# Kernel tuning notes

Measured on AMD Instinct MI355X. Metric: run time of the kernel, lower is better.

Reference implementation:

```python
import jax, jax.numpy as jnp
import numpy as np

B, V, K, DIN, H, DH, OBS, HID = 2048, 3, 32, 256, 8, 64, 128, 256
REP = H * DH
EPS = 1e-6


def _ln(x, g, b):
    mu = x.mean(-1, keepdims=True)
    var = ((x - mu) ** 2).mean(-1, keepdims=True)
    return (x - mu) * jax.lax.rsqrt(var + 1e-5) * g + b


def setup_inputs() -> dict:
    key = jax.random.key(0)
    ks = iter(jax.random.split(key, 32))
    nrm = lambda shape, s=0.05: jax.random.normal(next(ks), shape, jnp.float32) * s
    return {
        'x_anchor': jax.random.normal(next(ks), (B, V, DIN), jnp.float32),
        'x_neighbors': jax.random.normal(next(ks), (B, V, K, DIN), jnp.float32),
        'edge_weights': jax.random.uniform(next(ks), (B, V, K), jnp.float32),
        'g': jax.random.normal(next(ks), (B, OBS), jnp.float32),
        'aW': nrm((V, DIN, REP)), 'ab': jnp.zeros((V, REP)), 'ag': jnp.ones((V, REP)), 'abeta': jnp.zeros((V, REP)),
        'nW': nrm((V, DIN, REP)), 'nb': jnp.zeros((V, REP)), 'ng': jnp.ones((V, REP)), 'nbeta': jnp.zeros((V, REP)),
        'Wq': nrm((V, H, DH, DH)), 'Wk': nrm((V, H, DH, DH)), 'Wv': nrm((V, H, DH, DH)), 'Wo': nrm((V, H, DH, DH)),
        'geom_log_scale': jnp.zeros((V, H)),
        'cWq': nrm((H, DH, DH)), 'cWk': nrm((H, DH, DH)), 'cWv': nrm((H, DH, DH)), 'cWo': nrm((H, DH, DH)),
        'rW1': nrm((OBS, HID)), 'rb1': jnp.zeros((HID,)),
        'rW2': nrm((HID, HID)), 'rb2': jnp.zeros((HID,)),
        'vW': nrm((HID, H * V)), 'vb': jnp.zeros((H * V,)),
        'mW': nrm((HID, H)), 'mb': jnp.zeros((H,)),
        'gW': nrm((HID, H)), 'gb': jnp.zeros((H,)),
    }


def reference(x_anchor, x_neighbors, edge_weights, g, aW, ab, ag, abeta, nW, nb, ng, nbeta,
              Wq, Wk, Wv, Wo, geom_log_scale, cWq, cWk, cWv, cWo,
              rW1, rb1, rW2, rb2, vW, vb, mW, mb, gW, gb):
    # --- per-view encoders (vectorized over V with a leading v axis) ---
    ha = _ln(jnp.einsum('bvi,vio->bvo', x_anchor, aW) + ab, ag, abeta).reshape(B, V, H, DH)
    hn = _ln(jnp.einsum('bvki,vio->bvko', x_neighbors, nW) + nb[:, None, :],
             ng[:, None, :], nbeta[:, None, :]).reshape(B, V, K, H, DH)
    q = jnp.einsum('bvhd,vhde->bvhe', ha, Wq)
    k = jnp.einsum('bvkhd,vhde->bvkhe', hn, Wk)
    vv = jnp.einsum('bvkhd,vhde->bvkhe', hn, Wv)
    sc = jnp.einsum('bvhd,bvkhd->bvhk', q, k) / np.sqrt(DH).astype(np.float32)
    geom = jax.nn.softplus(geom_log_scale)  # [V,H]
    sc = sc + geom[None, :, :, None] * jnp.log(edge_weights[:, :, None, :] + EPS)
    attn = jax.nn.softmax(sc, axis=-1)
    ho = jnp.einsum('bvhk,bvkhd->bvhd', attn, vv)
    ho = jnp.einsum('bvhd,vhde->bvhe', ho, Wo) + ha  # residual
    view_tokens = jnp.transpose(ho, (0, 2, 1, 3))  # [B,H,V,Dh]
    # --- router ---
    hid = jax.nn.gelu(jnp.dot(g, rW1) + rb1, approximate=False)
    hid = jax.nn.gelu(jnp.dot(hid, rW2) + rb2, approximate=False)
    pi = jax.nn.softmax((jnp.dot(hid, vW) + vb).reshape(B, H, V), axis=-1)
    beta = jax.nn.sigmoid((jnp.dot(hid, mW) + mb)[..., None])  # [B,H,1]
    gate = jax.nn.softmax(jnp.dot(hid, gW) + gb, axis=-1)      # [B,H]
    # --- pi-weighted mixture + cross-view interaction with log-pi prior ---
    mix = jnp.einsum('bhv,bhvd->bhd', pi, view_tokens)
    qc = jnp.einsum('bhd,hde->bhe', mix, cWq)
    kc = jnp.einsum('bhvd,hde->bhve', view_tokens, cWk)
    vc = jnp.einsum('bhvd,hde->bhve', view_tokens, cWv)
    s2 = jnp.einsum('bhd,bhvd->bhv', qc, kc) / np.sqrt(DH).astype(np.float32) + jnp.log(pi + EPS)
    a2 = jax.nn.softmax(s2, axis=-1)
    cr = jnp.einsum('bhv,bhvd->bhd', a2, vc)
    cr = jnp.einsum('bhd,hde->bhe', cr, cWo)
    # mode blend + head gating; head_repr kept unflattened [B,H,Dh]
    return gate[..., None] * (beta * cr + (1.0 - beta) * mix)
```

## Files before the change

### kernel.cpp

```cpp
#include <hip/hip_runtime.h>

#define B_   2048
#define V_   3
#define K_   32
#define DIN_ 256
#define H_   8
#define DH_  64
#define REP_ 512

typedef unsigned short u16;
typedef unsigned int   u32;
typedef __bf16 bf8 __attribute__((ext_vector_type(8)));
typedef float  f4  __attribute__((ext_vector_type(4)));

static __device__ __forceinline__ u16 f2bf(float f) {
  union { float f; u32 i; } x; x.f = f;
  u32 r = (x.i + 0x7FFFu + ((x.i >> 16) & 1u)) >> 16;
  return (u16)r;
}
static __device__ __forceinline__ float bf2f(u16 u) {
  union { u32 i; float f; } x; x.i = ((u32)u) << 16;
  return x.f;
}

__global__ __launch_bounds__(256) void k0_prep(
    const float* __restrict__ nW, const float* __restrict__ aW,
    const float* __restrict__ Wk, const float* __restrict__ Wv,
    u16* __restrict__ nWt, u16* __restrict__ aWt,
    u16* __restrict__ Wkt, u16* __restrict__ Wvt)
{
  int id = blockIdx.x * 256 + threadIdx.x;
  if (id < 393216) {
    int v  = id / 131072, r  = id % 131072;
    int kt = r / 16384,   r2 = r % 16384;
    int n  = r2 / 32,     kk = r2 % 32;
    int src = (v * 256 + kt * 32 + kk) * 512 + n;
    nWt[id] = f2bf(nW[src]);
    aWt[id] = f2bf(aW[src]);
  } else {
    int j = id - 393216;
    int vh = j / 4096, r = j % 4096;
    int e = r / 64, d = r % 64;
    int src = (vh * 64 + d) * 64 + e;
    Wkt[j] = f2bf(Wk[src]);
    Wvt[j] = f2bf(Wv[src]);
  }
}

union K1Smem {
  struct { u16 A[64 * 256]; u16 Bt[512 * 32]; } p1;
  u16 S[64 * 512];
};

__global__ __launch_bounds__(512, 4) void k1_gemm_ln(
    const float* __restrict__ X,
    const u16*   __restrict__ Wt,
    const float* __restrict__ bias,
    const float* __restrict__ gamma,
    const float* __restrict__ betap,
    u16*   __restrict__ hn,
    float* __restrict__ ha,
    int mode, int b0, int Bc)
{
  __shared__ K1Smem sm;
  const int v = blockIdx.y, blk = blockIdx.x, t = threadIdx.x;

  {
    int row = t >> 3;
    int cbase = (t & 7) * 32;
    long grow;
    if (mode == 0) { int b = b0 + blk * 2 + (row >> 5); grow = ((long)(b * 3 + v) * 32 + (row & 31)) * 256; }
    else           { int b = blk * 64 + row;            grow = (long)(b * 3 + v) * 256; }
    const float4* src = (const float4*)(X + grow + cbase);
    int sw = row & 7;
    #pragma unroll
    for (int j = 0; j < 8; ++j) {
      float4 f = src[j];
      int col = cbase + j * 4;
      int c = col >> 3, m = col & 7;
      ushort4 u;
      u.x = f2bf(f.x); u.y = f2bf(f.y); u.z = f2bf(f.z); u.w = f2bf(f.w);
      *(ushort4*)&sm.p1.A[row * 256 + ((c ^ sw) << 3) + m] = u;
    }
  }

  const int w = t >> 6, l = t & 63, lm = l & 15, lg = l >> 4;
  const int wm = w & 1, wn = w >> 1;
  f4 acc[2][8];
  #pragma unroll
  for (int i = 0; i < 2; ++i)
    #pragma unroll
    for (int j = 0; j < 8; ++j) { f4 z = {0.f, 0.f, 0.f, 0.f}; acc[i][j] = z; }

  for (int kt = 0; kt < 8; ++kt) {
    __syncthreads();
    {
      const uint4* gsrc = (const uint4*)(Wt + (long)(v * 8 + kt) * 16384);
      #pragma unroll
      for (int r2 = 0; r2 < 4; ++r2) {
        int idx = r2 * 512 + t;
        uint4 d = gsrc[idx];
        int n = idx >> 2, c = idx & 3;
        int s = c ^ ((n >> 1) & 3);
        *(uint4*)&sm.p1.Bt[n * 32 + s * 8] = d;
      }
    }
    __syncthreads();
    bf8 af[2];
    #pragma unroll
    for (int tm = 0; tm < 2; ++tm) {
      int row = wm * 32 + tm * 16 + lm;
      int c = kt * 4 + lg;
      af[tm] = *(const bf8*)&sm.p1.A[row * 256 + ((c ^ (row & 7)) << 3)];
    }
    #pragma unroll
    for (int tn = 0; tn < 8; ++tn) {
      int n = wn * 128 + tn * 16 + lm;
      int s = lg ^ ((n >> 1) & 3);
      bf8 bv = *(const bf8*)&sm.p1.Bt[n * 32 + s * 8];
      acc[0][tn] = __builtin_amdgcn_mfma_f32_16x16x32_bf16(af[0], bv, acc[0][tn], 0, 0, 0);
      acc[1][tn] = __builtin_amdgcn_mfma_f32_16x16x32_bf16(af[1], bv, acc[1][tn], 0, 0, 0);
    }
  }
  __syncthreads();

  {
    float bcol[8];
    #pragma unroll
    for (int tn = 0; tn < 8; ++tn) bcol[tn] = bias[v * 512 + wn * 128 + tn * 16 + lm];
    #pragma unroll
    for (int tm = 0; tm < 2; ++tm)
      #pragma unroll
      for (int tn = 0; tn < 8; ++tn) {
        int col = wn * 128 + tn * 16 + lm;
        int c = col >> 3, m = col & 7;
        #pragma unroll
        for (int r = 0; r < 4; ++r) {
          int row = wm * 32 + tm * 16 + lg * 4 + r;
          sm.S[row * 512 + ((c ^ (row & 7)) << 3) + m] = f2bf(acc[tm][tn][r] + bcol[tn]);
        }
      }
  }
  __syncthreads();

  {
    int row = t >> 3, ch = t & 7, sw = row & 7;
    float vals[8][8];
    float s1 = 0.f, s2 = 0.f;
    #pragma unroll
    for (int j = 0; j < 8; ++j) {
      int c = j * 8 + ch;
      const u16* p8 = &sm.S[row * 512 + ((c ^ sw) << 3)];
      #pragma unroll
      for (int m = 0; m < 8; ++m) { float x = bf2f(p8[m]); vals[j][m] = x; s1 += x; s2 += x * x; }
    }
    #pragma unroll
    for (int d = 1; d < 8; d <<= 1) { s1 += __shfl_xor(s1, d, 64); s2 += __shfl_xor(s2, d, 64); }
    float mu = s1 * (1.f / 512.f);
    float var = s2 * (1.f / 512.f) - mu * mu;
    float rs = rsqrtf(var + 1e-5f);
    if (mode == 0) {
      int bl_ = blk * 2 + (row >> 5);
      int k = row & 31;
      #pragma unroll
      for (int j = 0; j < 8; ++j) {
        int col0 = j * 64 + ch * 8;
        float4 g0 = *(const float4*)&gamma[v * 512 + col0];
        float4 g1 = *(const float4*)&gamma[v * 512 + col0 + 4];
        float4 e0 = *(const float4*)&betap[v * 512 + col0];
        float4 e1 = *(const float4*)&betap[v * 512 + col0 + 4];
        u32 pk0 = (u32)f2bf((vals[j][0] - mu) * rs * g0.x + e0.x) |
                  ((u32)f2bf((vals[j][1] - mu) * rs * g0.y + e0.y) << 16);
        u32 pk1 = (u32)f2bf((vals[j][2] - mu) * rs * g0.z + e0.z) |
                  ((u32)f2bf((vals[j][3] - mu) * rs * g0.w + e0.w) << 16);
        u32 pk2 = (u32)f2bf((vals[j][4] - mu) * rs * g1.x + e1.x) |
                  ((u32)f2bf((vals[j][5] - mu) * rs * g1.y + e1.y) << 16);
        u32 pk3 = (u32)f2bf((vals[j][6] - mu) * rs * g1.z + e1.z) |
                  ((u32)f2bf((vals[j][7] - mu) * rs * g1.w + e1.w) << 16);
        uint4 q4; q4.x = pk0; q4.y = pk1; q4.z = pk2; q4.w = pk3;
        u16* dst = hn + (((long)(v * 8 + j) * Bc + bl_) * 32 + k) * 64 + ch * 8;
        *(uint4*)dst = q4;
      }
    } else {
      int b = blk * 64 + row;
      float* dst = ha + (long)(b * 3 + v) * 512;
      #pragma unroll
      for (int j = 0; j < 8; ++j) {
        int col0 = j * 64 + ch * 8;
        float4 g0 = *(const float4*)&gamma[v * 512 + col0];
        float4 g1 = *(const float4*)&gamma[v * 512 + col0 + 4];
        float4 e0 = *(const float4*)&betap[v * 512 + col0];
        float4 e1 = *(const float4*)&betap[v * 512 + col0 + 4];
        float4 w0, w1;
        w0.x = (vals[j][0] - mu) * rs * g0.x + e0.x;
        w0.y = (vals[j][1] - mu) * rs * g0.y + e0.y;
        w0.z = (vals[j][2] - mu) * rs * g0.z + e0.z;
        w0.w = (vals[j][3] - mu) * rs * g0.w + e0.w;
        w1.x = (vals[j][4] - mu) * rs * g1.x + e1.x;
        w1.y = (vals[j][5] - mu) * rs * g1.y + e1.y;
        w1.z = (vals[j][6] - mu) * rs * g1.z + e1.z;
        w1.w = (vals[j][7] - mu) * rs * g1.w + e1.w;
        *(float4*)&dst[col0] = w0;
        *(float4*)&dst[col0 + 4] = w1;
      }
    }
  }
}

__global__ __launch_bounds__(256, 2) void k2_attn(
    const u16*   __restrict__ hn,
    const float* __restrict__ ha,
    const u16*   __restrict__ Wkt,
    const u16*   __restrict__ Wvt,
    const float* __restrict__ Wq,
    const float* __restrict__ Wo,
    const float* __restrict__ ew,
    const float* __restrict__ gls,
    float* __restrict__ vt,
    int b0, int Bc)
{
  const int v = blockIdx.z, h = blockIdx.y;
  const int bL0 = blockIdx.x * 8;
  const int t = threadIdx.x;
  __shared__ u16 A[256 * 72];
  __shared__ u16 Wk_s[64 * 72], Wv_s[64 * 72];
  __shared__ float q_s[8 * 64], ha_s[8 * 64], attn_s[8 * 32], o_s[8 * 64];

  {
    const uint4* src = (const uint4*)(hn + ((long)(v * 8 + h) * Bc + bL0) * 2048);
    #pragma unroll
    for (int i = 0; i < 8; ++i) {
      uint4 d = src[t * 8 + i];
      *(uint4*)&A[t * 72 + i * 8] = d;
    }
  }
  {
    const uint4* sk = (const uint4*)(Wkt + (long)(v * 8 + h) * 4096);
    const uint4* sv = (const uint4*)(Wvt + (long)(v * 8 + h) * 4096);
    #pragma unroll
    for (int i = 0; i < 2; ++i) {
      int idx = i * 256 + t;
      int n = idx >> 3, k8 = (idx & 7) * 8;
      *(uint4*)&Wk_s[n * 72 + k8] = sk[idx];
      *(uint4*)&Wv_s[n * 72 + k8] = sv[idx];
    }
  }
  #pragma unroll
  for (int i = 0; i < 2; ++i) {
    int idx = i * 256 + t; int b = idx >> 6, e = idx & 63;
    ha_s[idx] = ha[((long)(b0 + bL0 + b) * 3 + v) * 512 + h * 64 + e];
  }
  __syncthreads();

  const int w = t >> 6, l = t & 63, lm = l & 15, lg = l >> 4;
  f4 aK[4][4], aV[4][4];
  #pragma unroll
  for (int i = 0; i < 4; ++i)
    #pragma unroll
    for (int j = 0; j < 4; ++j) { f4 z = {0.f, 0.f, 0.f, 0.f}; aK[i][j] = z; aV[i][j] = z; }

  #pragma unroll
  for (int ks = 0; ks < 2; ++ks) {
    int ko = ks * 32 + lg * 8;
    bf8 af[4];
    #pragma unroll
    for (int tm = 0; tm < 4; ++tm) af[tm] = *(const bf8*)&A[(w * 64 + tm * 16 + lm) * 72 + ko];
    #pragma unroll
    for (int tn = 0; tn < 4; ++tn) {
      bf8 bk = *(const bf8*)&Wk_s[(tn * 16 + lm) * 72 + ko];
      bf8 bv = *(const bf8*)&Wv_s[(tn * 16 + lm) * 72 + ko];
      #pragma unroll
      for (int tm = 0; tm < 4; ++tm) {
        aK[tm][tn] = __builtin_amdgcn_mfma_f32_16x16x32_bf16(af[tm], bk, aK[tm][tn], 0, 0, 0);
        aV[tm][tn] = __builtin_amdgcn_mfma_f32_16x16x32_bf16(af[tm], bv, aV[tm][tn], 0, 0, 0);
      }
    }
  }
  __syncthreads();

  #pragma unroll
  for (int tm = 0; tm < 4; ++tm)
    #pragma unroll
    for (int tn = 0; tn < 4; ++tn)
      #pragma unroll
      for (int r = 0; r < 4; ++r) {
        int row = w * 64 + tm * 16 + lg * 4 + r;
        int col = tn * 16 + lm;
        A[row * 72 + col] = f2bf(aK[tm][tn][r]);
      }
  {
    const float* wq = Wq + (long)(v * 8 + h) * 4096;
    #pragma unroll
    for (int i = 0; i < 2; ++i) {
      int idx = i * 256 + t; int b = idx >> 6, e = idx & 63;
      float acc = 0.f;
      for (int d = 0; d < 64; ++d) acc += ha_s[b * 64 + d] * wq[d * 64 + e];
      q_s[idx] = acc * 0.125f;
    }
  }
  __syncthreads();

  {
    int b = t >> 5, k = t & 31;
    float x = gls[v * 8 + h];
    float gsc = (x > 20.f) ? x : log1pf(expf(x));
    float s = 0.f;
    const u16* kr = &A[(b * 32 + k) * 72];
    for (int d = 0; d < 64; ++d) s += q_s[b * 64 + d] * bf2f(kr[d]);
    float e_w = ew[((long)(b0 + bL0 + b) * 3 + v) * 32 + k];
    s += gsc * logf(e_w + 1e-6f);
    float m = s;
    #pragma unroll
    for (int d = 1; d < 32; d <<= 1) m = fmaxf(m, __shfl_xor(m, d, 64));
    float exs = expf(s - m), sum = exs;
    #pragma unroll
    for (int d = 1; d < 32; d <<= 1) sum += __shfl_xor(sum, d, 64);
    attn_s[b * 32 + k] = exs / sum;
  }
  __syncthreads();

  {
    float p[2][4] = {{0.f,0.f,0.f,0.f},{0.f,0.f,0.f,0.f}};
    #pragma unroll
    for (int tm = 0; tm < 4; ++tm) {
      int bh = tm >> 1;
      #pragma unroll
      for (int r = 0; r < 4; ++r) {
        int k = (tm & 1) * 16 + lg * 4 + r;
        float a = attn_s[(w * 2 + bh) * 32 + k];
        #pragma unroll
        for (int tn = 0; tn < 4; ++tn) p[bh][tn] += a * aV[tm][tn][r];
      }
    }
    #pragma unroll
    for (int bh = 0; bh < 2; ++bh)
      #pragma unroll
      for (int tn = 0; tn < 4; ++tn) {
        float x = p[bh][tn];
        x += __shfl_xor(x, 16, 64);
        x += __shfl_xor(x, 32, 64);
        if (l < 16) o_s[(w * 2 + bh) * 64 + tn * 16 + lm] = x;
      }
  }
  __syncthreads();

  {
    const float* wo = Wo + (long)(v * 8 + h) * 4096;
    #pragma unroll
    for (int i = 0; i < 2; ++i) {
      int idx = i * 256 + t; int b = idx >> 6, e = idx & 63;
      float acc = ha_s[b * 64 + e];
      for (int d = 0; d < 64; ++d) acc += o_s[b * 64 + d] * wo[d * 64 + e];
      vt[(((long)(b0 + bL0 + b) * 8 + h) * 3 + v) * 64 + e] = acc;
    }
  }
}

__global__ __launch_bounds__(256) void k3_router(
    const float* __restrict__ g, const float* __restrict__ rW1, const float* __restrict__ rb1,
    const float* __restrict__ rW2, const float* __restrict__ rb2,
    const float* __restrict__ vW, const float* __restrict__ vb,
    const float* __restrict__ mW, const float* __restrict__ mb,
    const float* __restrict__ gW, const float* __restrict__ gb,
    float* __restrict__ pi, float* __restrict__ beta_o, float* __restrict__ gate_o)
{
  __shared__ float gs[16 * 128], h1[16 * 256], h2[16 * 256], lgt[16 * 40];
  int t = threadIdx.x, bb = blockIdx.x * 16;
  #pragma unroll
  for (int r = 0; r < 8; ++r) { int idx = r * 256 + t; gs[idx] = g[(long)bb * 128 + idx]; }
  __syncthreads();
  {
    int bl = t >> 4, e0 = (t & 15) * 16;
    float acc[16];
    #pragma unroll
    for (int j = 0; j < 16; ++j) acc[j] = rb1[e0 + j];
    for (int i = 0; i < 128; ++i) {
      float gv = gs[bl * 128 + i];
      const float* wr = rW1 + i * 256 + e0;
      #pragma unroll
      for (int j = 0; j < 16; ++j) acc[j] += gv * wr[j];
    }
    #pragma unroll
    for (int j = 0; j < 16; ++j) { float x = acc[j]; h1[bl * 256 + e0 + j] = 0.5f * x * (1.f + erff(x * 0.70710678118f)); }
  }
  __syncthreads();
  {
    int bl = t >> 4, e0 = (t & 15) * 16;
    float acc[16];
    #pragma unroll
    for (int j = 0; j < 16; ++j) acc[j] = rb2[e0 + j];
    for (int i = 0; i < 256; ++i) {
      float hv = h1[bl * 256 + i];
      const float* wr = rW2 + i * 256 + e0;
      #pragma unroll
      for (int j = 0; j < 16; ++j) acc[j] += hv * wr[j];
    }
    #pragma unroll
    for (int j = 0; j < 16; ++j) { float x = acc[j]; h2[bl * 256 + e0 + j] = 0.5f * x * (1.f + erff(x * 0.70710678118f)); }
  }
  __syncthreads();
  for (int idx = t; idx < 640; idx += 256) {
    int bl = idx / 40, j = idx % 40;
    const float* W; float bs; int col, stride;
    if (j < 24)      { W = vW; col = j;      stride = 24; bs = vb[j]; }
    else if (j < 32) { W = mW; col = j - 24; stride = 8;  bs = mb[j - 24]; }
    else             { W = gW; col = j - 32; stride = 8;  bs = gb[j - 32]; }
    float acc = bs;
    for (int i = 0; i < 256; ++i) acc += h2[bl * 256 + i] * W[i * stride + col];
    lgt[bl * 40 + j] = acc;
  }
  __syncthreads();
  if (t < 16) {
    int b = bb + t;
    const float* L = &lgt[t * 40];
    #pragma unroll
    for (int hh = 0; hh < 8; ++hh) {
      float a0 = L[hh * 3], a1 = L[hh * 3 + 1], a2v = L[hh * 3 + 2];
      float m = fmaxf(a0, fmaxf(a1, a2v));
      float x0 = expf(a0 - m), x1 = expf(a1 - m), x2 = expf(a2v - m);
      float inv = 1.f / (x0 + x1 + x2);
      pi[b * 24 + hh * 3 + 0] = x0 * inv;
      pi[b * 24 + hh * 3 + 1] = x1 * inv;
      pi[b * 24 + hh * 3 + 2] = x2 * inv;
      beta_o[b * 8 + hh] = 1.f / (1.f + expf(-L[24 + hh]));
    }
    float m = L[32];
    #pragma unroll
    for (int hh = 1; hh < 8; ++hh) m = fmaxf(m, L[32 + hh]);
    float s = 0.f, ex[8];
    #pragma unroll
    for (int hh = 0; hh < 8; ++hh) { ex[hh] = expf(L[32 + hh] - m); s += ex[hh]; }
    float inv = 1.f / s;
    #pragma unroll
    for (int hh = 0; hh < 8; ++hh) gate_o[b * 8 + hh] = ex[hh] * inv;
  }
}

__global__ __launch_bounds__(256) void k4_cross(
    const float* __restrict__ vtg, const float* __restrict__ pig,
    const float* __restrict__ betag, const float* __restrict__ gateg,
    const float* __restrict__ cWq, const float* __restrict__ cWk,
    const float* __restrict__ cWv, const float* __restrict__ cWo,
    float* __restrict__ out)
{
  __shared__ float smem[12544];
  float* vts   = smem;
  float* mixs  = smem + 6144;
  float* buf1  = smem + 8192;
  float* buf2  = smem + 10240;
  float* a2s   = smem + 12288;
  float* pis   = smem + 12384;
  float* betas = smem + 12480;
  float* gates = smem + 12512;

  int t = threadIdx.x, bblk = blockIdx.x * 4;
  {
    const float4* src = (const float4*)(vtg + (long)bblk * 1536);
    #pragma unroll
    for (int r = 0; r < 6; ++r) ((float4*)vts)[r * 256 + t] = src[r * 256 + t];
    if (t < 96) pis[t] = pig[bblk * 24 + t];
    if (t < 32) { betas[t] = betag[bblk * 8 + t]; gates[t] = gateg[bblk * 8 + t]; }
  }
  __syncthreads();
  int bl = t >> 6, hh = (t >> 3) & 7, e0 = (t & 7) * 8;
  const float* vbh = &vts[(bl * 8 + hh) * 192];
  {
    float p0 = pis[bl * 24 + hh * 3], p1 = pis[bl * 24 + hh * 3 + 1], p2 = pis[bl * 24 + hh * 3 + 2];
    #pragma unroll
    for (int j = 0; j < 8; ++j) {
      int e = e0 + j;
      mixs[(bl * 8 + hh) * 64 + e] = p0 * vbh[e] + p1 * vbh[64 + e] + p2 * vbh[128 + e];
    }
  }
  __syncthreads();
  {
    float acc[8] = {0.f,0.f,0.f,0.f,0.f,0.f,0.f,0.f};
    const float* M = &mixs[(bl * 8 + hh) * 64];
    for (int d = 0; d < 64; ++d) {
      float mv = M[d];
      const float* wr = &cWq[(hh * 64 + d) * 64 + e0];
      #pragma unroll
      for (int j = 0; j < 8; ++j) acc[j] += mv * wr[j];
    }
    #pragma unroll
    for (int j = 0; j < 8; ++j) buf1[(bl * 8 + hh) * 64 + e0 + j] = acc[j] * 0.125f;
  }
  __syncthreads();
  {
    const float* Q = &buf1[(bl * 8 + hh) * 64];
    #pragma unroll
    for (int d2 = 0; d2 < 8; ++d2) {
      const float* wr = &cWk[(hh * 64 + e0 + d2) * 64];
      float a = 0.f;
      for (int e = 0; e < 64; ++e) a += wr[e] * Q[e];
      buf2[(bl * 8 + hh) * 64 + e0 + d2] = a;
    }
  }
  __syncthreads();
  if (t < 32) {
    int b2 = t >> 3, h2 = t & 7;
    const float* Wd = &buf2[(b2 * 8 + h2) * 64];
    const float* vb2 = &vts[(b2 * 8 + h2) * 192];
    float s[3];
    #pragma unroll
    for (int v3 = 0; v3 < 3; ++v3) {
      float a = 0.f;
      for (int d = 0; d < 64; ++d) a += Wd[d] * vb2[v3 * 64 + d];
      s[v3] = a + logf(pis[b2 * 24 + h2 * 3 + v3] + 1e-6f);
    }
    float m = fmaxf(s[0], fmaxf(s[1], s[2]));
    float x0 = expf(s[0] - m), x1 = expf(s[1] - m), x2 = expf(s[2] - m);
    float inv = 1.f / (x0 + x1 + x2);
    a2s[(b2 * 8 + h2) * 3 + 0] = x0 * inv;
    a2s[(b2 * 8 + h2) * 3 + 1] = x1 * inv;
    a2s[(b2 * 8 + h2) * 3 + 2] = x2 * inv;
  }
  __syncthreads();
  {
    float a0 = a2s[(bl * 8 + hh) * 3], a1 = a2s[(bl * 8 + hh) * 3 + 1], a2v = a2s[(bl * 8 + hh) * 3 + 2];
    #pragma unroll
    for (int j = 0; j < 8; ++j) {
      int e = e0 + j;
      buf1[(bl * 8 + hh) * 64 + e] = a0 * vbh[e] + a1 * vbh[64 + e] + a2v * vbh[128 + e];
    }
  }
  __syncthreads();
  {
    float acc[8] = {0.f,0.f,0.f,0.f,0.f,0.f,0.f,0.f};
    const float* Y = &buf1[(bl * 8 + hh) * 64];
    for (int d = 0; d < 64; ++d) {
      float yv = Y[d];
      const float* wr = &cWv[(hh * 64 + d) * 64 + e0];
      #pragma unroll
      for (int j = 0; j < 8; ++j) acc[j] += yv * wr[j];
    }
    #pragma unroll
    for (int j = 0; j < 8; ++j) buf2[(bl * 8 + hh) * 64 + e0 + j] = acc[j];
  }
  __syncthreads();
  {
    float acc[8] = {0.f,0.f,0.f,0.f,0.f,0.f,0.f,0.f};
    const float* C2 = &buf2[(bl * 8 + hh) * 64];
    for (int d = 0; d < 64; ++d) {
      float cv = C2[d];
      const float* wr = &cWo[(hh * 64 + d) * 64 + e0];
      #pragma unroll
      for (int j = 0; j < 8; ++j) acc[j] += cv * wr[j];
    }
    float bt = betas[bl * 8 + hh], gt = gates[bl * 8 + hh];
    const float* M = &mixs[(bl * 8 + hh) * 64];
    #pragma unroll
    for (int j = 0; j < 8; ++j)
      out[((long)(bblk + bl) * 8 + hh) * 64 + e0 + j] = gt * (bt * acc[j] + (1.f - bt) * M[e0 + j]);
  }
}

extern "C" void kernel_launch(void* const* d_in, const int* in_sizes, int n_in,
                              void* d_out, int out_size, void* d_ws, size_t ws_size,
                              hipStream_t stream) {
  const float* x_anchor    = (const float*)d_in[0];
  const float* x_neighbors = (const float*)d_in[1];
  const float* edge_w      = (const float*)d_in[2];
  const float* g           = (const float*)d_in[3];
  const float* aW  = (const float*)d_in[4];
  const float* ab  = (const float*)d_in[5];
  const float* ag  = (const float*)d_in[6];
  const float* abeta = (const float*)d_in[7];
  const float* nW  = (const float*)d_in[8];
  const float* nb  = (const float*)d_in[9];
  const float* ng  = (const float*)d_in[10];
  const float* nbeta = (const float*)d_in[11];
  const float* Wq  = (const float*)d_in[12];
  const float* Wk  = (const float*)d_in[13];
  const float* Wv  = (const float*)d_in[14];
  const float* Wo  = (const float*)d_in[15];
  const float* gls = (const float*)d_in[16];
  const float* cWq = (const float*)d_in[17];
  const float* cWk = (const float*)d_in[18];
  const float* cWv = (const float*)d_in[19];
  const float* cWo = (const float*)d_in[20];
  const float* rW1 = (const float*)d_in[21];
  const float* rb1 = (const float*)d_in[22];
  const float* rW2 = (const float*)d_in[23];
  const float* rb2 = (const float*)d_in[24];
  const float* vW  = (const float*)d_in[25];
  const float* vb  = (const float*)d_in[26];
  const float* mW  = (const float*)d_in[27];
  const float* mb  = (const float*)d_in[28];
  const float* gW  = (const float*)d_in[29];
  const float* gb  = (const float*)d_in[30];

  char* p = (char*)d_ws;
  u16* nWt = (u16*)p;  p += 786432;
  u16* aWt = (u16*)p;  p += 786432;
  u16* Wkt = (u16*)p;  p += 196608;
  u16* Wvt = (u16*)p;  p += 196608;
  float* ha   = (float*)p; p += 12582912;
  float* vtb  = (float*)p; p += 12582912;
  float* pib  = (float*)p; p += 196608;
  float* betb = (float*)p; p += 65536;
  float* gatb = (float*)p; p += 65536;
  size_t fixed = (size_t)(p - (char*)d_ws);
  int C = 1;
  while (C < 128 && fixed + (size_t)(2048 / C) * 98304 > ws_size) C <<= 1;
  int Bc = 2048 / C;
  u16* hnb = (u16*)p;

  k0_prep<<<1920, 256, 0, stream>>>(nW, aW, Wk, Wv, nWt, aWt, Wkt, Wvt);
  k1_gemm_ln<<<dim3(32, 3), 512, 0, stream>>>(x_anchor, aWt, ab, ag, abeta,
                                              (u16*)nullptr, ha, 1, 0, Bc);
  k3_router<<<128, 256, 0, stream>>>(g, rW1, rb1, rW2, rb2, vW, vb, mW, mb, gW, gb,
                                     pib, betb, gatb);
  for (int c = 0; c < C; ++c) {
    int b0 = c * Bc;
    k1_gemm_ln<<<dim3(Bc / 2, 3), 512, 0, stream>>>(x_neighbors, nWt, nb, ng, nbeta,
                                                    hnb, (float*)nullptr, 0, b0, Bc);
    k2_attn<<<dim3(Bc / 8, 8, 3), 256, 0, stream>>>(hnb, ha, Wkt, Wvt, Wq, Wo,
                                                    edge_w, gls, vtb, b0, Bc);
  }
  k4_cross<<<512, 256, 0, stream>>>(vtb, pib, betb, gatb, cWq, cWk, cWv, cWo,
                                    (float*)d_out);
}
```

Measured before the change: 864.5 us.

## Load GEMM B operand directly from global and halve k1 shared memory

The k1 GEMM+LayerNorm kernel now reads the transposed weight fragments straight from global memory (L2-resident) into registers instead of staging them through shared memory with two barriers per k-step. The LayerNorm epilogue reuses the 32 KB A buffer in two passes of 32 rows, so shared memory per block drops from 64 KB to 32 KB, which may allow more resident blocks. The costs are global-latency-bound B loads inside the k loop, with no LDS reuse across the two wm warps, plus extra barriers and a second LDS read in the epilogue.

```diff
diff --git a/kernel.cpp b/kernel.cpp
--- a/kernel.cpp
+++ b/kernel.cpp
@@ -47,11 +47,6 @@
   }
 }
 
-union K1Smem {
-  struct { u16 A[64 * 256]; u16 Bt[512 * 32]; } p1;
-  u16 S[64 * 512];
-};
-
 __global__ __launch_bounds__(512, 4) void k1_gemm_ln(
     const float* __restrict__ X,
     const u16*   __restrict__ Wt,
@@ -62,7 +57,7 @@
     float* __restrict__ ha,
     int mode, int b0, int Bc)
 {
-  __shared__ K1Smem sm;
+  __shared__ u16 sA[64 * 256];
   const int v = blockIdx.y, blk = blockIdx.x, t = threadIdx.x;
 
   {
@@ -80,9 +75,10 @@
       int c = col >> 3, m = col & 7;
       ushort4 u;
       u.x = f2bf(f.x); u.y = f2bf(f.y); u.z = f2bf(f.z); u.w = f2bf(f.w);
-      *(ushort4*)&sm.p1.A[row * 256 + ((c ^ sw) << 3) + m] = u;
-    }
-  }
+      *(ushort4*)&sA[row * 256 + ((c ^ sw) << 3) + m] = u;
+    }
+  }
+  __syncthreads();
 
   const int w = t >> 6, l = t & 63, lm = l & 15, lg = l >> 4;
   const int wm = w & 1, wn = w >> 1;
@@ -93,117 +89,100 @@
     for (int j = 0; j < 8; ++j) { f4 z = {0.f, 0.f, 0.f, 0.f}; acc[i][j] = z; }
 
   for (int kt = 0; kt < 8; ++kt) {
-    __syncthreads();
-    {
-      const uint4* gsrc = (const uint4*)(Wt + (long)(v * 8 + kt) * 16384);
-      #pragma unroll
-      for (int r2 = 0; r2 < 4; ++r2) {
-        int idx = r2 * 512 + t;
-        uint4 d = gsrc[idx];
-        int n = idx >> 2, c = idx & 3;
-        int s = c ^ ((n >> 1) & 3);
-        *(uint4*)&sm.p1.Bt[n * 32 + s * 8] = d;
-      }
-    }
-    __syncthreads();
+    const u16* bbase = Wt + ((long)(v * 8 + kt) * 512 + wn * 128 + lm) * 32 + lg * 8;
+    bf8 bv[8];
+    #pragma unroll
+    for (int tn = 0; tn < 8; ++tn)
+      bv[tn] = *(const bf8*)(bbase + tn * 512);
     bf8 af[2];
     #pragma unroll
     for (int tm = 0; tm < 2; ++tm) {
       int row = wm * 32 + tm * 16 + lm;
       int c = kt * 4 + lg;
-      af[tm] = *(const bf8*)&sm.p1.A[row * 256 + ((c ^ (row & 7)) << 3)];
+      af[tm] = *(const bf8*)&sA[row * 256 + ((c ^ (row & 7)) << 3)];
     }
     #pragma unroll
     for (int tn = 0; tn < 8; ++tn) {
-      int n = wn * 128 + tn * 16 + lm;
-      int s = lg ^ ((n >> 1) & 3);
-      bf8 bv = *(const bf8*)&sm.p1.Bt[n * 32 + s * 8];
-      acc[0][tn] = __builtin_amdgcn_mfma_f32_16x16x32_bf16(af[0], bv, acc[0][tn], 0, 0, 0);
-      acc[1][tn] = __builtin_amdgcn_mfma_f32_16x16x32_bf16(af[1], bv, acc[1][tn], 0, 0, 0);
-    }
-  }
-  __syncthreads();
-
-  {
-    float bcol[8];
-    #pragma unroll
-    for (int tn = 0; tn < 8; ++tn) bcol[tn] = bias[v * 512 + wn * 128 + tn * 16 + lm];
-    #pragma unroll
-    for (int tm = 0; tm < 2; ++tm)
-      #pragma unroll
-      for (int tn = 0; tn < 8; ++tn) {
-        int col = wn * 128 + tn * 16 + lm;
-        int c = col >> 3, m = col & 7;
+      acc[0][tn] = __builtin_amdgcn_mfma_f32_16x16x32_bf16(af[0], bv[tn], acc[0][tn], 0, 0, 0);
+      acc[1][tn] = __builtin_amdgcn_mfma_f32_16x16x32_bf16(af[1], bv[tn], acc[1][tn], 0, 0, 0);
+    }
+  }
+  __syncthreads();
+
+  u16* S = sA;
+  #pragma unroll
+  for (int p = 0; p < 2; ++p) {
+    if (wm == p) {
+      float bcol[8];
+      #pragma unroll
+      for (int tn = 0; tn < 8; ++tn) bcol[tn] = bias[v * 512 + wn * 128 + tn * 16 + lm];
+      #pragma unroll
+      for (int tm = 0; tm < 2; ++tm)
         #pragma unroll
-        for (int r = 0; r < 4; ++r) {
-          int row = wm * 32 + tm * 16 + lg * 4 + r;
-          sm.S[row * 512 + ((c ^ (row & 7)) << 3) + m] = f2bf(acc[tm][tn][r] + bcol[tn]);
+        for (int tn = 0; tn < 8; ++tn) {
+          int col = wn * 128 + tn * 16 + lm;
+          int c = col >> 3, m = col & 7;
+          #pragma unroll
+          for (int r = 0; r < 4; ++r) {
+            int row = tm * 16 + lg * 4 + r;
+            S[row * 512 + ((c ^ (row & 7)) << 3) + m] = f2bf(acc[tm][tn][r] + bcol[tn]);
+          }
         }
+    }
+    __syncthreads();
+    {
+      int row = t >> 4, ch = t & 15, sw = row & 7;
+      float s1 = 0.f, s2 = 0.f;
+      #pragma unroll
+      for (int j = 0; j < 4; ++j) {
+        int c = j * 16 + ch;
+        const u16* p8 = &S[row * 512 + ((c ^ sw) << 3)];
+        #pragma unroll
+        for (int m = 0; m < 8; ++m) { float x = bf2f(p8[m]); s1 += x; s2 += x * x; }
       }
-  }
-  __syncthreads();
-
-  {
-    int row = t >> 3, ch = t & 7, sw = row & 7;
-    float vals[8][8];
-    float s1 = 0.f, s2 = 0.f;
-    #pragma unroll
-    for (int j = 0; j < 8; ++j) {
-      int c = j * 8 + ch;
-      const u16* p8 = &sm.S[row * 512 + ((c ^ sw) << 3)];
-      #pragma unroll
-      for (int m = 0; m < 8; ++m) { float x = bf2f(p8[m]); vals[j][m] = x; s1 += x; s2 += x * x; }
-    }
-    #pragma unroll
-    for (int d = 1; d < 8; d <<= 1) { s1 += __shfl_xor(s1, d, 64); s2 += __shfl_xor(s2, d, 64); }
-    float mu = s1 * (1.f / 512.f);
-    float var = s2 * (1.f / 512.f) - mu * mu;
-    float rs = rsqrtf(var + 1e-5f);
-    if (mode == 0) {
-      int bl_ = blk * 2 + (row >> 5);
-      int k = row & 31;
-      #pragma unroll
-      for (int j = 0; j < 8; ++j) {
-        int col0 = j * 64 + ch * 8;
+      #pragma unroll
+      for (int d = 1; d < 16; d <<= 1) { s1 += __shfl_xor(s1, d, 64); s2 += __shfl_xor(s2, d, 64); }
+      float mu = s1 * (1.f / 512.f);
+      float var = s2 * (1.f / 512.f) - mu * mu;
+      float rs = rsqrtf(var + 1e-5f);
+      #pragma unroll
+      for (int j = 0; j < 4; ++j) {
+        int c = j * 16 + ch;
+        const u16* p8 = &S[row * 512 + ((c ^ sw) << 3)];
+        int col0 = c * 8;
         float4 g0 = *(const float4*)&gamma[v * 512 + col0];
         float4 g1 = *(const float4*)&gamma[v * 512 + col0 + 4];
         float4 e0 = *(const float4*)&betap[v * 512 + col0];
         float4 e1 = *(const float4*)&betap[v * 512 + col0 + 4];
-        u32 pk0 = (u32)f2bf((vals[j][0] - mu) * rs * g0.x + e0.x) |
-                  ((u32)f2bf((vals[j][1] - mu) * rs * g0.y + e0.y) << 16);
-        u32 pk1 = (u32)f2bf((vals[j][2] - mu) * rs * g0.z + e0.z) |
-                  ((u32)f2bf((vals[j][3] - mu) * rs * g0.w + e0.w) << 16);
-        u32 pk2 = (u32)f2bf((vals[j][4] - mu) * rs * g1.x + e1.x) |
-                  ((u32)f2bf((vals[j][5] - mu) * rs * g1.y + e1.y) << 16);
-        u32 pk3 = (u32)f2bf((vals[j][6] - mu) * rs * g1.z + e1.z) |
-                  ((u32)f2bf((vals[j][7] - mu) * rs * g1.w + e1.w) << 16);
-        uint4 q4; q4.x = pk0; q4.y = pk1; q4.z = pk2; q4.w = pk3;
-        u16* dst = hn + (((long)(v * 8 + j) * Bc + bl_) * 32 + k) * 64 + ch * 8;
-        *(uint4*)dst = q4;
+        float y0 = (bf2f(p8[0]) - mu) * rs * g0.x + e0.x;
+        float y1 = (bf2f(p8[1]) - mu) * rs * g0.y + e0.y;
+        float y2 = (bf2f(p8[2]) - mu) * rs * g0.z + e0.z;
+        float y3 = (bf2f(p8[3]) - mu) * rs * g0.w + e0.w;
+        float y4 = (bf2f(p8[4]) - mu) * rs * g1.x + e1.x;
+        float y5 = (bf2f(p8[5]) - mu) * rs * g1.y + e1.y;
+        float y6 = (bf2f(p8[6]) - mu) * rs * g1.z + e1.z;
+        float y7 = (bf2f(p8[7]) - mu) * rs * g1.w + e1.w;
+        if (mode == 0) {
+          int head = c >> 3, eo = (c & 7) * 8;
+          uint4 q4;
+          q4.x = (u32)f2bf(y0) | ((u32)f2bf(y1) << 16);
+          q4.y = (u32)f2bf(y2) | ((u32)f2bf(y3) << 16);
+          q4.z = (u32)f2bf(y4) | ((u32)f2bf(y5) << 16);
+          q4.w = (u32)f2bf(y6) | ((u32)f2bf(y7) << 16);
+          u16* dst = hn + (((long)(v * 8 + head) * Bc + (blk * 2 + p)) * 32 + row) * 64 + eo;
+          *(uint4*)dst = q4;
+        } else {
+          int b = blk * 64 + p * 32 + row;
+          float* dst = ha + (long)(b * 3 + v) * 512 + col0;
+          float4 w0, w1;
+          w0.x = y0; w0.y = y1; w0.z = y2; w0.w = y3;
+          w1.x = y4; w1.y = y5; w1.z = y6; w1.w = y7;
+          *(float4*)dst = w0;
+          *(float4*)(dst + 4) = w1;
+        }
       }
-    } else {
-      int b = blk * 64 + row;
-      float* dst = ha + (long)(b * 3 + v) * 512;
-      #pragma unroll
-      for (int j = 0; j < 8; ++j) {
-        int col0 = j * 64 + ch * 8;
-        float4 g0 = *(const float4*)&gamma[v * 512 + col0];
-        float4 g1 = *(const float4*)&gamma[v * 512 + col0 + 4];
-        float4 e0 = *(const float4*)&betap[v * 512 + col0];
-        float4 e1 = *(const float4*)&betap[v * 512 + col0 + 4];
-        float4 w0, w1;
-        w0.x = (vals[j][0] - mu) * rs * g0.x + e0.x;
-        w0.y = (vals[j][1] - mu) * rs * g0.y + e0.y;
-        w0.z = (vals[j][2] - mu) * rs * g0.z + e0.z;
-        w0.w = (vals[j][3] - mu) * rs * g0.w + e0.w;
-        w1.x = (vals[j][4] - mu) * rs * g1.x + e1.x;
-        w1.y = (vals[j][5] - mu) * rs * g1.y + e1.y;
-        w1.z = (vals[j][6] - mu) * rs * g1.z + e1.z;
-        w1.w = (vals[j][7] - mu) * rs * g1.w + e1.w;
-        *(float4*)&dst[col0] = w0;
-        *(float4*)&dst[col0 + 4] = w1;
-      }
-    }
+    }
+    __syncthreads();
   }
 }
 
```

Result: slower. 945.2 us (+9.3%).
